# Kernel tuning notes

Measured on AMD Instinct MI355X. Metric: run time of the kernel, lower is better.

## Reference

```python
import jax, jax.numpy as jnp
import numpy as np

N = 8192
FEAT = 128
HID = 128
EMB = 128
NHEADS = 2
RO_HID = 256
G_EMB = 128
ALPHA = 0.2          # LeakyReLU negative slope
NEG_INF = -9e15      # matches -9000000000000000.0 in the torch source


def _xavier(k, shape, gain=1.0):
    fan_in, fan_out = shape[-2], shape[-1]
    s = gain * np.sqrt(2.0 / (fan_in + fan_out))
    return jax.random.normal(k, shape, jnp.float32) * jnp.float32(s)


def setup_inputs() -> dict:
    key = jax.random.key(0)
    ks = jax.random.split(key, 10)
    adj = jax.random.randint(ks[0], (N, N), 0, 2, jnp.int32)          # dense 0/1 adjacency
    x = jax.random.normal(ks[1], (N, FEAT), jnp.float32)
    W_heads = _xavier(ks[2], (NHEADS, FEAT, HID), gain=1.414)
    a_heads = _xavier(ks[3], (NHEADS, 2 * HID, 1), gain=1.414)
    W_out = _xavier(ks[4], (NHEADS * HID, EMB), gain=1.414)
    a_out = _xavier(ks[5], (2 * EMB, 1), gain=1.414)
    ge_w1 = _xavier(ks[6], (FEAT + EMB, RO_HID))
    ge_b1 = jnp.zeros((RO_HID,), jnp.float32)
    ge_w2 = _xavier(ks[7], (RO_HID, G_EMB))
    ge_b2 = jnp.zeros((G_EMB,), jnp.float32)
    return dict(adj=adj, feature_matrix=x, W_heads=W_heads, a_heads=a_heads,
                W_out=W_out, a_out=a_out, ge_w1=ge_w1, ge_b1=ge_b1,
                ge_w2=ge_w2, ge_b2=ge_b2, supply=0)


def _gat_layer(x, mask, W, a, concat):
    # Faithful to GraphAttentionLayer: e_ij = leakyrelu([Wh_i || Wh_j] @ a).
    # The concat-then-matmul decomposes exactly as Wh@a[:F] + (Wh@a[F:])^T,
    # avoiding the O(N^2 * 2F) a_input tensor while computing identical math.
    Wh = x @ W                                   # [N, F]
    F_out = W.shape[1]
    f1 = (Wh @ a[:F_out]).squeeze(-1)            # [N]
    f2 = (Wh @ a[F_out:]).squeeze(-1)            # [N]
    e = jax.nn.leaky_relu(f1[:, None] + f2[None, :], ALPHA)   # [N, N]
    e = jnp.where(mask, e, jnp.float32(NEG_INF))
    att = jax.nn.softmax(e, axis=1)              # dropout is identity in eval mode
    h = att @ Wh                                 # [N, F]
    return jax.nn.elu(h) if concat else h


def reference(adj, feature_matrix, W_heads, a_heads, W_out, a_out,
              ge_w1, ge_b1, ge_w2, ge_b2, supply):
    mask = adj > 0
    # GAT: multi-head layer 1 (concat), then out_att (no concat) + elu
    heads = [_gat_layer(feature_matrix, mask, W_heads[i], a_heads[i], True)
             for i in range(NHEADS)]
    h = jnp.concatenate(heads, axis=1)           # [N, NHEADS*HID]
    node_emb = jax.nn.elu(_gat_layer(h, mask, W_out, a_out, False))  # [N, EMB]
    # GraphEmb readout (mode='mean')
    combined = jnp.concatenate([feature_matrix, node_emb], axis=1)   # [N, FEAT+EMB]
    h1 = jax.nn.relu(combined @ ge_w1 + ge_b1)
    h2 = jax.nn.relu(h1 @ ge_w2 + ge_b2)
    graph_emb = jnp.mean(h2, axis=0)             # [G_EMB]
    return node_emb, graph_emb
```

## Files before the change

kernel.cpp:

```cpp
#include <hip/hip_runtime.h>

typedef unsigned short u16;
typedef __attribute__((ext_vector_type(4))) float f32x4;
typedef __attribute__((ext_vector_type(8))) short bf16x8;
typedef __attribute__((ext_vector_type(4))) unsigned short u16x4;
typedef __attribute__((ext_vector_type(4))) float float4v;

#define N 8192

__device__ __forceinline__ float bf2f(u16 u){
  union { float f; unsigned int i; } v; v.i = ((unsigned int)u) << 16; return v.f;
}
__device__ __forceinline__ u16 f2bf(float f){
  union { float f; unsigned int i; } v; v.f = f;
  unsigned int r = v.i + 0x7fffu + ((v.i >> 16) & 1u);
  return (u16)(r >> 16);
}
__device__ __forceinline__ f32x4 mfma16(bf16x8 a, bf16x8 b, f32x4 c){
  return __builtin_amdgcn_mfma_f32_16x16x32_bf16(a, b, c, 0, 0, 0);
}

__global__ __launch_bounds__(256) void k_pack(const int* __restrict__ adj,
                                              unsigned long long* __restrict__ packed){
  const int wid = blockIdx.x * 4 + (threadIdx.x >> 6);
  const int lane = threadIdx.x & 63;
  const size_t base = (size_t)wid * 128;
  for (int g = 0; g < 128; ++g){
    const size_t grp = base + g;
    const int v = adj[grp * 64 + lane];
    const unsigned long long mask = __ballot(v != 0);
    if (lane == 0) packed[grp] = mask;
  }
}

__global__ void k_split_x(const float* __restrict__ x, u16* __restrict__ hi, u16* __restrict__ lo){
  const int idx = blockIdx.x * 256 + threadIdx.x;
  float4v v = ((const float4v*)x)[idx];
  u16x4 h, l;
  #pragma unroll
  for (int e = 0; e < 4; ++e){ u16 hb = f2bf(v[e]); h[e] = hb; l[e] = f2bf(v[e] - bf2f(hb)); }
  ((u16x4*)hi)[idx] = h; ((u16x4*)lo)[idx] = l;
}

template<bool SPLIT>
__global__ void k_transpose(const float* __restrict__ src, u16* __restrict__ dhi,
                            u16* __restrict__ dlo, int K, int Ncols){
  const size_t boff = (size_t)blockIdx.y * K * Ncols;
  const int idx = blockIdx.x * 256 + threadIdx.x;
  if (idx >= K * Ncols) return;
  const int n = idx / K, k = idx % K;
  const float v = src[boff + (size_t)k * Ncols + n];
  const u16 h = f2bf(v);
  dhi[boff + idx] = h;
  if constexpr (SPLIT) dlo[boff + idx] = f2bf(v - bf2f(h));
}

__global__ __launch_bounds__(64) void k_gemm_at(
    const u16* __restrict__ Ahi, const u16* __restrict__ Alo,
    const u16* __restrict__ Bhi, const u16* __restrict__ Blo,
    u16* __restrict__ outT,
    const float* __restrict__ avec,
    float* __restrict__ f1, float* __restrict__ f2,
    int K)
{
  const int head = blockIdx.z;
  Ahi += (size_t)head * 128 * K; Alo += (size_t)head * 128 * K;
  outT += (size_t)head * 128 * N;
  avec += (size_t)head * 256;
  f1 += (size_t)head * N; f2 += (size_t)head * N;
  const int lane = threadIdx.x & 63;
  const int r16 = lane & 15, g4 = lane >> 4;
  const int cg = blockIdx.y;
  const size_t ib = (size_t)blockIdx.x * 128;
  f32x4 acc[8];
  #pragma unroll
  for (int it = 0; it < 8; ++it) acc[it] = (f32x4){0.f, 0.f, 0.f, 0.f};
  for (int kk = 0; kk < K; kk += 32){
    bf16x8 ah = *(const bf16x8*)(Ahi + (size_t)(cg * 16 + r16) * K + kk + g4 * 8);
    bf16x8 al = *(const bf16x8*)(Alo + (size_t)(cg * 16 + r16) * K + kk + g4 * 8);
    #pragma unroll
    for (int it = 0; it < 8; ++it){
      const size_t boff = (ib + it * 16 + r16) * (size_t)K + kk + g4 * 8;
      bf16x8 bh = *(const bf16x8*)(Bhi + boff);
      bf16x8 bl = *(const bf16x8*)(Blo + boff);
      acc[it] = mfma16(ah, bh, acc[it]);
      acc[it] = mfma16(ah, bl, acc[it]);
      acc[it] = mfma16(al, bh, acc[it]);
    }
  }
  float a1v[4], a2v[4];
  #pragma unroll
  for (int q = 0; q < 4; ++q){
    a1v[q] = avec[cg * 16 + g4 * 4 + q];
    a2v[q] = avec[128 + cg * 16 + g4 * 4 + q];
  }
  #pragma unroll
  for (int it = 0; it < 8; ++it){
    float p1 = 0.f, p2 = 0.f;
    #pragma unroll
    for (int q = 0; q < 4; ++q){
      float v = acc[it][q];
      outT[(size_t)(cg * 16 + g4 * 4 + q) * N + ib + it * 16 + r16] = f2bf(v);
      p1 += v * a1v[q]; p2 += v * a2v[q];
    }
    p1 += __shfl_xor(p1, 16); p1 += __shfl_xor(p1, 32);
    p2 += __shfl_xor(p2, 16); p2 += __shfl_xor(p2, 32);
    if (lane < 16){
      atomicAdd(&f1[ib + it * 16 + lane], p1);
      atomicAdd(&f2[ib + it * 16 + lane], p2);
    }
  }
}

template<int RG, bool L2OUT>
__global__ __launch_bounds__(256) void k_attn(
    const unsigned char* __restrict__ pk,
    const u16* __restrict__ whT_all,
    const float* __restrict__ f1_all, const float* __restrict__ f2_all,
    u16* __restrict__ out_hi, u16* __restrict__ out_lo,
    float* __restrict__ out_f32, u16* __restrict__ comb)
{
  constexpr int ROWS = RG * 16;
  __shared__ float smO[3][ROWS][132];
  __shared__ float smM[3][ROWS];
  __shared__ float smL[3][ROWS];

  const int h = blockIdx.y;
  const u16* whT = whT_all + (size_t)h * 128 * N;
  const float* f1 = f1_all + (size_t)h * N;
  const float* f2 = f2_all + (size_t)h * N;
  const int seg = threadIdx.x >> 6;
  const int lane = threadIdx.x & 63;
  const int r16 = lane & 15, g4 = lane >> 4;
  const size_t ibase = (size_t)blockIdx.x * ROWS;

  float m[RG], l[RG], f1v[RG];
  f32x4 acc[RG][8];
  #pragma unroll
  for (int rg = 0; rg < RG; ++rg){
    m[rg] = -3e38f; l[rg] = 0.f;
    f1v[rg] = f1[ibase + rg * 16 + r16];
    #pragma unroll
    for (int ct = 0; ct < 8; ++ct) acc[rg][ct] = (f32x4){0.f, 0.f, 0.f, 0.f};
  }

  for (int t = seg; t < 128; t += 4){
    const int j0 = t * 64;
    bf16x8 bfr[2][8];
    #pragma unroll
    for (int kk = 0; kk < 2; ++kk)
      #pragma unroll
      for (int ct = 0; ct < 8; ++ct)
        bfr[kk][ct] = *(const bf16x8*)(whT + (size_t)(ct * 16 + r16) * N + j0 + kk * 32 + g4 * 8);
    float4v f2a = *(const float4v*)(f2 + j0 + g4 * 8);
    float4v f2b = *(const float4v*)(f2 + j0 + g4 * 8 + 4);
    float4v f2c = *(const float4v*)(f2 + j0 + 32 + g4 * 8);
    float4v f2d = *(const float4v*)(f2 + j0 + 32 + g4 * 8 + 4);
    float f2v[16] = {f2a[0],f2a[1],f2a[2],f2a[3], f2b[0],f2b[1],f2b[2],f2b[3],
                     f2c[0],f2c[1],f2c[2],f2c[3], f2d[0],f2d[1],f2d[2],f2d[3]};
    unsigned int bits[RG][2];
    #pragma unroll
    for (int rg = 0; rg < RG; ++rg){
      const size_t rb = (ibase + rg * 16 + r16) * 1024 + (j0 >> 3);
      bits[rg][0] = pk[rb + g4];
      bits[rg][1] = pk[rb + 4 + g4];
    }
    #pragma unroll
    for (int rg = 0; rg < RG; ++rg){
      float e[16]; float tmax = -3e38f;
      #pragma unroll
      for (int kk = 0; kk < 2; ++kk)
        #pragma unroll
        for (int x = 0; x < 8; ++x){
          float s = f1v[rg] + f2v[kk * 8 + x];
          s = (s > 0.f) ? s : 0.2f * s;
          s = ((bits[rg][kk] >> x) & 1u) ? s : -3e38f;
          e[kk * 8 + x] = s; tmax = fmaxf(tmax, s);
        }
      tmax = fmaxf(tmax, __shfl_xor(tmax, 16));
      tmax = fmaxf(tmax, __shfl_xor(tmax, 32));
      const float mold = m[rg];
      const float mnew = fmaxf(mold, tmax);
      m[rg] = mnew;
      float psum = 0.f;
      u16 pb[16];
      #pragma unroll
      for (int kk = 0; kk < 2; ++kk)
        #pragma unroll
        for (int x = 0; x < 8; ++x){
          float p = ((bits[rg][kk] >> x) & 1u) ? __expf(e[kk * 8 + x] - mnew) : 0.f;
          psum += p;
          pb[kk * 8 + x] = f2bf(p);
        }
      psum += __shfl_xor(psum, 16);
      psum += __shfl_xor(psum, 32);
      const float sc = __expf(mold - mnew);
      l[rg] = l[rg] * sc + psum;
      if (__any(mnew != mold)){
        float s0 = __shfl(sc, g4 * 4 + 0), s1 = __shfl(sc, g4 * 4 + 1);
        float s2 = __shfl(sc, g4 * 4 + 2), s3 = __shfl(sc, g4 * 4 + 3);
        f32x4 sv = {s0, s1, s2, s3};
        #pragma unroll
        for (int ct = 0; ct < 8; ++ct) acc[rg][ct] *= sv;
      }
      bf16x8 a0, a1;
      #pragma unroll
      for (int x = 0; x < 8; ++x){ a0[x] = (short)pb[x]; a1[x] = (short)pb[8 + x]; }
      #pragma unroll
      for (int ct = 0; ct < 8; ++ct){
        acc[rg][ct] = mfma16(a0, bfr[0][ct], acc[rg][ct]);
        acc[rg][ct] = mfma16(a1, bfr[1][ct], acc[rg][ct]);
      }
    }
  }
  if (seg > 0){
    #pragma unroll
    for (int rg = 0; rg < RG; ++rg){
      #pragma unroll
      for (int ct = 0; ct < 8; ++ct)
        #pragma unroll
        for (int q = 0; q < 4; ++q)
          smO[seg - 1][rg * 16 + g4 * 4 + q][ct * 16 + r16] = acc[rg][ct][q];
      if (lane < 16){ smM[seg - 1][rg * 16 + lane] = m[rg]; smL[seg - 1][rg * 16 + lane] = l[rg]; }
    }
  }
  __syncthreads();
  if (seg == 0){
    #pragma unroll
    for (int rg = 0; rg < RG; ++rg){
      #pragma unroll
      for (int q = 0; q < 4; ++q){
        const int r = rg * 16 + g4 * 4 + q;
        const float m0 = __shfl(m[rg], g4 * 4 + q);
        const float l0 = __shfl(l[rg], g4 * 4 + q);
        const float mm = fmaxf(fmaxf(m0, smM[0][r]), fmaxf(smM[1][r], smM[2][r]));
        const float w0 = __expf(m0 - mm);
        const float w1 = __expf(smM[0][r] - mm);
        const float w2 = __expf(smM[1][r] - mm);
        const float w3 = __expf(smM[2][r] - mm);
        const float L = w0 * l0 + w1 * smL[0][r] + w2 * smL[1][r] + w3 * smL[2][r];
        const float rinv = 1.f / L;
        #pragma unroll
        for (int ct = 0; ct < 8; ++ct){
          const int c = ct * 16 + r16;
          float val = w0 * acc[rg][ct][q] + w1 * smO[0][r][c] + w2 * smO[1][r][c] + w3 * smO[2][r][c];
          float o = val * rinv;
          o = (o > 0.f) ? o : (__expf(o) - 1.f);
          const size_t i = ibase + r;
          if constexpr (!L2OUT){
            const u16 hb = f2bf(o);
            out_hi[i * 256 + (size_t)h * 128 + c] = hb;
            out_lo[i * 256 + (size_t)h * 128 + c] = f2bf(o - bf2f(hb));
          } else {
            out_f32[i * 128 + c] = o;
            comb[i * 256 + 128 + c] = f2bf(o);
          }
        }
      }
    }
  }
}

__global__ void k_copyx(const float* __restrict__ x, u16* __restrict__ comb){
  const int idx = blockIdx.x * 256 + threadIdx.x;
  const int i = idx >> 5;
  const int c4 = (idx & 31) * 4;
  float4v v = *(const float4v*)(x + (size_t)i * 128 + c4);
  u16x4 hv;
  #pragma unroll
  for (int e = 0; e < 4; ++e) hv[e] = f2bf(v[e]);
  *(u16x4*)(comb + (size_t)i * 256 + c4) = hv;
}

template<bool STORE, bool COLSUM>
__global__ __launch_bounds__(256) void k_gemm_row(
    const u16* __restrict__ A,
    const u16* __restrict__ BT,
    const float* __restrict__ bias,
    u16* __restrict__ out, float* __restrict__ csum,
    int K, int Ntot)
{
  const int lane = threadIdx.x & 63, w = threadIdx.x >> 6;
  const int r16 = lane & 15, g4 = lane >> 4;
  const size_t rbase = (size_t)blockIdx.x * 64 + w * 16;
  const int cbase = blockIdx.y * 128;
  f32x4 acc[8];
  #pragma unroll
  for (int ct = 0; ct < 8; ++ct) acc[ct] = (f32x4){0.f, 0.f, 0.f, 0.f};
  for (int kk = 0; kk < K; kk += 32){
    bf16x8 af = *(const bf16x8*)(A + (rbase + r16) * (size_t)K + kk + g4 * 8);
    #pragma unroll
    for (int ct = 0; ct < 8; ++ct){
      bf16x8 bfr = *(const bf16x8*)(BT + (size_t)(cbase + ct * 16 + r16) * K + kk + g4 * 8);
      acc[ct] = mfma16(af, bfr, acc[ct]);
    }
  }
  #pragma unroll
  for (int ct = 0; ct < 8; ++ct){
    const float bv = bias[cbase + ct * 16 + r16];
    float s = 0.f;
    #pragma unroll
    for (int q = 0; q < 4; ++q){
      float v = acc[ct][q] + bv;
      v = fmaxf(v, 0.f);
      if constexpr (STORE)
        out[(rbase + g4 * 4 + q) * (size_t)Ntot + cbase + ct * 16 + r16] = f2bf(v);
      s += v;
    }
    if constexpr (COLSUM){
      s += __shfl_xor(s, 16); s += __shfl_xor(s, 32);
      if (lane < 16) atomicAdd(&csum[cbase + ct * 16 + lane], s);
    }
  }
}

__global__ void k_final(const float* __restrict__ csum, float* __restrict__ out){
  out[threadIdx.x] = csum[threadIdx.x] * (1.f / 8192.f);
}

extern "C" void kernel_launch(void* const* d_in, const int* in_sizes, int n_in,
                              void* d_out, int out_size, void* d_ws, size_t ws_size,
                              hipStream_t stream) {
  const int*   adj = (const int*)d_in[0];
  const float* x   = (const float*)d_in[1];
  const float* Wh  = (const float*)d_in[2];
  const float* ah  = (const float*)d_in[3];
  const float* Wo  = (const float*)d_in[4];
  const float* ao  = (const float*)d_in[5];
  const float* g1  = (const float*)d_in[6];
  const float* b1  = (const float*)d_in[7];
  const float* g2  = (const float*)d_in[8];
  const float* b2  = (const float*)d_in[9];
  float* outp = (float*)d_out;
  char* ws = (char*)d_ws;

  const size_t PK   = 0;
  const size_t WHT1 = 8388608;
  const size_t FV   = 12582912;
  const size_t F1A  = FV;
  const size_t F2A  = FV + 65536;
  const size_t F1B  = FV + 131072;
  const size_t F2B  = FV + 163840;
  const size_t HHI  = 12779520;
  const size_t HLO  = 16973824;
  const size_t WHT2 = 21168128;
  const size_t XHI  = 23265280;
  const size_t XLO  = 25362432;
  const size_t CSUM = 27459584;
  const size_t WTHH = 27460096;
  const size_t WTHL = 27525632;
  const size_t WOTH = 27591168;
  const size_t WOTL = 27656704;
  const size_t G1T  = 27722240;
  const size_t G2T  = 27853312;
  const size_t H1   = PK;
  const size_t COMB = WHT1;

  hipMemsetAsync(ws + FV, 0, 196608, stream);
  hipMemsetAsync(ws + CSUM, 0, 512, stream);

  k_pack<<<2048, 256, 0, stream>>>(adj, (unsigned long long*)(ws + PK));
  k_split_x<<<1024, 256, 0, stream>>>(x, (u16*)(ws + XHI), (u16*)(ws + XLO));
  k_transpose<true ><<<dim3(64, 2), 256, 0, stream>>>(Wh, (u16*)(ws + WTHH), (u16*)(ws + WTHL), 128, 128);
  k_transpose<true ><<<dim3(128, 1), 256, 0, stream>>>(Wo, (u16*)(ws + WOTH), (u16*)(ws + WOTL), 256, 128);
  k_transpose<false><<<dim3(256, 1), 256, 0, stream>>>(g1, (u16*)(ws + G1T), nullptr, 256, 256);
  k_transpose<false><<<dim3(128, 1), 256, 0, stream>>>(g2, (u16*)(ws + G2T), nullptr, 256, 128);

  k_gemm_at<<<dim3(64, 8, 2), 64, 0, stream>>>(
      (const u16*)(ws + WTHH), (const u16*)(ws + WTHL),
      (const u16*)(ws + XHI),  (const u16*)(ws + XLO),
      (u16*)(ws + WHT1), ah, (float*)(ws + F1A), (float*)(ws + F2A), 128);

  k_attn<2, false><<<dim3(256, 2), 256, 0, stream>>>(
      (const unsigned char*)(ws + PK), (const u16*)(ws + WHT1),
      (const float*)(ws + F1A), (const float*)(ws + F2A),
      (u16*)(ws + HHI), (u16*)(ws + HLO), nullptr, nullptr);

  k_gemm_at<<<dim3(64, 8, 1), 64, 0, stream>>>(
      (const u16*)(ws + WOTH), (const u16*)(ws + WOTL),
      (const u16*)(ws + HHI),  (const u16*)(ws + HLO),
      (u16*)(ws + WHT2), ao, (float*)(ws + F1B), (float*)(ws + F2B), 256);

  k_copyx<<<1024, 256, 0, stream>>>(x, (u16*)(ws + COMB));

  k_attn<1, true><<<dim3(512, 1), 256, 0, stream>>>(
      (const unsigned char*)(ws + PK), (const u16*)(ws + WHT2),
      (const float*)(ws + F1B), (const float*)(ws + F2B),
      nullptr, nullptr, outp, (u16*)(ws + COMB));

  k_gemm_row<true, false><<<dim3(128, 2), 256, 0, stream>>>(
      (const u16*)(ws + COMB), (const u16*)(ws + G1T), b1,
      (u16*)(ws + H1), nullptr, 256, 256);
  k_gemm_row<false, true><<<dim3(128, 1), 256, 0, stream>>>(
      (const u16*)(ws + H1), (const u16*)(ws + G2T), b2,
      nullptr, (float*)(ws + CSUM), 256, 128);
  k_final<<<1, 128, 0, stream>>>((const float*)(ws + CSUM), outp + (size_t)N * 128);
}
```

Before: 811.0 us.

## Use static softmax max bound, split-K attention with merge, drop hi/lo bf16 split

Attention logits are now computed as x·(W a) through small GEMV kernels in a log2 scale. The per-row softmax maximum is taken as an upper bound from leakyrelu(f1 + max f2), which removes online max tracking and accumulator rescaling. Attention is split over key segments across many small 64-thread blocks, and each segment writes bf16 partial outputs and row sums that a separate merge kernel combines, applying normalization and ELU. The hi/lo split bf16 GEMMs are replaced by plain bf16. This raises parallelism and removes the rescale work, but adds partial-buffer memory traffic, extra launches, and some loss of precision.

```diff
diff --git a/kernel.cpp b/kernel.cpp
--- a/kernel.cpp
+++ b/kernel.cpp
@@ -1,12 +1,13 @@
 #include <hip/hip_runtime.h>
+#include <hip/hip_bf16.h>
 
 typedef unsigned short u16;
 typedef __attribute__((ext_vector_type(4))) float f32x4;
 typedef __attribute__((ext_vector_type(8))) short bf16x8;
 typedef __attribute__((ext_vector_type(4))) unsigned short u16x4;
-typedef __attribute__((ext_vector_type(4))) float float4v;
 
 #define N 8192
+#define LOG2E 1.4426950408889634f
 
 __device__ __forceinline__ float bf2f(u16 u){
   union { float f; unsigned int i; } v; v.i = ((unsigned int)u) << 16; return v.f;
@@ -25,6 +26,7 @@
   const int wid = blockIdx.x * 4 + (threadIdx.x >> 6);
   const int lane = threadIdx.x & 63;
   const size_t base = (size_t)wid * 128;
+  #pragma unroll 4
   for (int g = 0; g < 128; ++g){
     const size_t grp = base + g;
     const int v = adj[grp * 64 + lane];
@@ -33,249 +35,280 @@
   }
 }
 
-__global__ void k_split_x(const float* __restrict__ x, u16* __restrict__ hi, u16* __restrict__ lo){
+__global__ __launch_bounds__(256) void k_x2bf(const float* __restrict__ x,
+                                              u16* __restrict__ xbf, u16* __restrict__ comb){
   const int idx = blockIdx.x * 256 + threadIdx.x;
-  float4v v = ((const float4v*)x)[idx];
-  u16x4 h, l;
-  #pragma unroll
-  for (int e = 0; e < 4; ++e){ u16 hb = f2bf(v[e]); h[e] = hb; l[e] = f2bf(v[e] - bf2f(hb)); }
-  ((u16x4*)hi)[idx] = h; ((u16x4*)lo)[idx] = l;
-}
-
-template<bool SPLIT>
-__global__ void k_transpose(const float* __restrict__ src, u16* __restrict__ dhi,
-                            u16* __restrict__ dlo, int K, int Ncols){
+  f32x4 v = ((const f32x4*)x)[idx];
+  u16x4 h;
+  #pragma unroll
+  for (int e = 0; e < 4; ++e) h[e] = f2bf(v[e]);
+  ((u16x4*)xbf)[idx] = h;
+  const int i = idx >> 5, c4 = (idx & 31) * 4;
+  *(u16x4*)(comb + (size_t)i * 256 + c4) = h;
+}
+
+__global__ void k_transpose(const float* __restrict__ src, u16* __restrict__ dst,
+                            int K, int Ncols){
   const size_t boff = (size_t)blockIdx.y * K * Ncols;
   const int idx = blockIdx.x * 256 + threadIdx.x;
   if (idx >= K * Ncols) return;
   const int n = idx / K, k = idx % K;
-  const float v = src[boff + (size_t)k * Ncols + n];
-  const u16 h = f2bf(v);
-  dhi[boff + idx] = h;
-  if constexpr (SPLIT) dlo[boff + idx] = f2bf(v - bf2f(h));
-}
-
-__global__ __launch_bounds__(64) void k_gemm_at(
-    const u16* __restrict__ Ahi, const u16* __restrict__ Alo,
-    const u16* __restrict__ Bhi, const u16* __restrict__ Blo,
-    u16* __restrict__ outT,
-    const float* __restrict__ avec,
-    float* __restrict__ f1, float* __restrict__ f2,
-    int K)
-{
-  const int head = blockIdx.z;
-  Ahi += (size_t)head * 128 * K; Alo += (size_t)head * 128 * K;
-  outT += (size_t)head * 128 * N;
-  avec += (size_t)head * 256;
-  f1 += (size_t)head * N; f2 += (size_t)head * N;
-  const int lane = threadIdx.x & 63;
+  dst[boff + idx] = f2bf(src[boff + (size_t)k * Ncols + n]);
+}
+
+__global__ __launch_bounds__(256) void k_wa(const float* __restrict__ Wh, const float* __restrict__ ah,
+                                            const float* __restrict__ Wo, const float* __restrict__ ao,
+                                            float* __restrict__ wa){
+  const int z = blockIdx.x, t = threadIdx.x;
+  if (z < 2){
+    if (t < 128){
+      float a1 = 0.f, a2 = 0.f;
+      for (int c = 0; c < 128; ++c){
+        const float w = Wh[(size_t)z * 16384 + t * 128 + c];
+        a1 += w * ah[z * 256 + c];
+        a2 += w * ah[z * 256 + 128 + c];
+      }
+      wa[z * 128 + t] = a1; wa[256 + z * 128 + t] = a2;
+    }
+  } else {
+    if (t < 256){
+      float a1 = 0.f, a2 = 0.f;
+      for (int c = 0; c < 128; ++c){
+        const float w = Wo[(size_t)t * 128 + c];
+        a1 += w * ao[c];
+        a2 += w * ao[128 + c];
+      }
+      wa[512 + t] = a1; wa[768 + t] = a2;
+    }
+  }
+}
+
+__global__ __launch_bounds__(256) void k_gemv1(const float* __restrict__ x, const float* __restrict__ wa,
+                                               float* __restrict__ f1s, float* __restrict__ f2s){
+  const int h = blockIdx.y;
+  const float* wa1 = wa + h * 128;
+  const float* wa2 = wa + 256 + h * 128;
+  const int lane = threadIdx.x & 63, w = threadIdx.x >> 6;
   const int r16 = lane & 15, g4 = lane >> 4;
-  const int cg = blockIdx.y;
-  const size_t ib = (size_t)blockIdx.x * 128;
-  f32x4 acc[8];
-  #pragma unroll
-  for (int it = 0; it < 8; ++it) acc[it] = (f32x4){0.f, 0.f, 0.f, 0.f};
+  const int row = blockIdx.x * 16 + w * 4 + g4;
+  const float* xr = x + (size_t)row * 128 + r16 * 8;
+  f32x4 x0 = *(const f32x4*)(xr);
+  f32x4 x1 = *(const f32x4*)(xr + 4);
+  f32x4 wA0 = *(const f32x4*)(wa1 + r16 * 8);
+  f32x4 wA1 = *(const f32x4*)(wa1 + r16 * 8 + 4);
+  f32x4 wB0 = *(const f32x4*)(wa2 + r16 * 8);
+  f32x4 wB1 = *(const f32x4*)(wa2 + r16 * 8 + 4);
+  float d1 = 0.f, d2 = 0.f;
+  #pragma unroll
+  for (int e = 0; e < 4; ++e){
+    d1 += x0[e] * wA0[e] + x1[e] * wA1[e];
+    d2 += x0[e] * wB0[e] + x1[e] * wB1[e];
+  }
+  d1 += __shfl_xor(d1, 1); d1 += __shfl_xor(d1, 2); d1 += __shfl_xor(d1, 4); d1 += __shfl_xor(d1, 8);
+  d2 += __shfl_xor(d2, 1); d2 += __shfl_xor(d2, 2); d2 += __shfl_xor(d2, 4); d2 += __shfl_xor(d2, 8);
+  if (r16 == 0){
+    f1s[(size_t)h * N + row] = d1 * LOG2E;
+    f2s[(size_t)h * N + row] = d2 * LOG2E;
+  }
+}
+
+__global__ __launch_bounds__(256) void k_gemv2(const u16* __restrict__ hbf,
+                                               const float* __restrict__ wao1, const float* __restrict__ wao2,
+                                               float* __restrict__ f1s, float* __restrict__ f2s){
+  const int lane = threadIdx.x & 63, w = threadIdx.x >> 6;
+  const int r16 = lane & 15, g4 = lane >> 4;
+  const int row = blockIdx.x * 16 + w * 4 + g4;
+  bf16x8 h0 = *(const bf16x8*)(hbf + (size_t)row * 256 + r16 * 16);
+  bf16x8 h1 = *(const bf16x8*)(hbf + (size_t)row * 256 + r16 * 16 + 8);
+  float d1 = 0.f, d2 = 0.f;
+  #pragma unroll
+  for (int e = 0; e < 8; ++e){
+    const float v0 = bf2f((u16)h0[e]), v1 = bf2f((u16)h1[e]);
+    d1 += v0 * wao1[r16 * 16 + e] + v1 * wao1[r16 * 16 + 8 + e];
+    d2 += v0 * wao2[r16 * 16 + e] + v1 * wao2[r16 * 16 + 8 + e];
+  }
+  d1 += __shfl_xor(d1, 1); d1 += __shfl_xor(d1, 2); d1 += __shfl_xor(d1, 4); d1 += __shfl_xor(d1, 8);
+  d2 += __shfl_xor(d2, 1); d2 += __shfl_xor(d2, 2); d2 += __shfl_xor(d2, 4); d2 += __shfl_xor(d2, 8);
+  if (r16 == 0){
+    f1s[row] = d1 * LOG2E;
+    f2s[row] = d2 * LOG2E;
+  }
+}
+
+__global__ __launch_bounds__(256) void k_fmax(const float* __restrict__ f2s, float* __restrict__ fmax){
+  const int h = blockIdx.x;
+  const float* f = f2s + (size_t)h * N;
+  float m = -3e38f;
+  for (int i = threadIdx.x; i < N; i += 256) m = fmaxf(m, f[i]);
+  m = fmaxf(m, __shfl_xor(m, 1));  m = fmaxf(m, __shfl_xor(m, 2));
+  m = fmaxf(m, __shfl_xor(m, 4));  m = fmaxf(m, __shfl_xor(m, 8));
+  m = fmaxf(m, __shfl_xor(m, 16)); m = fmaxf(m, __shfl_xor(m, 32));
+  __shared__ float sm[4];
+  if ((threadIdx.x & 63) == 0) sm[threadIdx.x >> 6] = m;
+  __syncthreads();
+  if (threadIdx.x == 0) fmax[h] = fmaxf(fmaxf(sm[0], sm[1]), fmaxf(sm[2], sm[3]));
+}
+
+__global__ __launch_bounds__(256) void k_gemm_at(const u16* __restrict__ A_all, const u16* __restrict__ B,
+                                                 u16* __restrict__ outT_all, int K){
+  const int head = blockIdx.y;
+  const u16* A = A_all + (size_t)head * 128 * K;
+  u16* outT = outT_all + (size_t)head * 128 * N;
+  const int lane = threadIdx.x & 63, w = threadIdx.x >> 6;
+  const int r16 = lane & 15, g4 = lane >> 4;
+  const size_t ib = (size_t)blockIdx.x * 128 + w * 32;
+  f32x4 acc[8][2];
+  #pragma unroll
+  for (int cg = 0; cg < 8; ++cg){ acc[cg][0] = (f32x4){0,0,0,0}; acc[cg][1] = (f32x4){0,0,0,0}; }
   for (int kk = 0; kk < K; kk += 32){
-    bf16x8 ah = *(const bf16x8*)(Ahi + (size_t)(cg * 16 + r16) * K + kk + g4 * 8);
-    bf16x8 al = *(const bf16x8*)(Alo + (size_t)(cg * 16 + r16) * K + kk + g4 * 8);
-    #pragma unroll
-    for (int it = 0; it < 8; ++it){
-      const size_t boff = (ib + it * 16 + r16) * (size_t)K + kk + g4 * 8;
-      bf16x8 bh = *(const bf16x8*)(Bhi + boff);
-      bf16x8 bl = *(const bf16x8*)(Blo + boff);
-      acc[it] = mfma16(ah, bh, acc[it]);
-      acc[it] = mfma16(ah, bl, acc[it]);
-      acc[it] = mfma16(al, bh, acc[it]);
-    }
-  }
-  float a1v[4], a2v[4];
-  #pragma unroll
-  for (int q = 0; q < 4; ++q){
-    a1v[q] = avec[cg * 16 + g4 * 4 + q];
-    a2v[q] = avec[128 + cg * 16 + g4 * 4 + q];
-  }
-  #pragma unroll
-  for (int it = 0; it < 8; ++it){
-    float p1 = 0.f, p2 = 0.f;
-    #pragma unroll
-    for (int q = 0; q < 4; ++q){
-      float v = acc[it][q];
-      outT[(size_t)(cg * 16 + g4 * 4 + q) * N + ib + it * 16 + r16] = f2bf(v);
-      p1 += v * a1v[q]; p2 += v * a2v[q];
-    }
-    p1 += __shfl_xor(p1, 16); p1 += __shfl_xor(p1, 32);
-    p2 += __shfl_xor(p2, 16); p2 += __shfl_xor(p2, 32);
-    if (lane < 16){
-      atomicAdd(&f1[ib + it * 16 + lane], p1);
-      atomicAdd(&f2[ib + it * 16 + lane], p2);
-    }
-  }
-}
-
-template<int RG, bool L2OUT>
-__global__ __launch_bounds__(256) void k_attn(
+    bf16x8 b0 = *(const bf16x8*)(B + (ib + r16) * (size_t)K + kk + g4 * 8);
+    bf16x8 b1 = *(const bf16x8*)(B + (ib + 16 + r16) * (size_t)K + kk + g4 * 8);
+    #pragma unroll
+    for (int cg = 0; cg < 8; ++cg){
+      bf16x8 a = *(const bf16x8*)(A + (size_t)(cg * 16 + r16) * K + kk + g4 * 8);
+      acc[cg][0] = mfma16(a, b0, acc[cg][0]);
+      acc[cg][1] = mfma16(a, b1, acc[cg][1]);
+    }
+  }
+  #pragma unroll
+  for (int cg = 0; cg < 8; ++cg)
+    #pragma unroll
+    for (int it = 0; it < 2; ++it)
+      #pragma unroll
+      for (int q = 0; q < 4; ++q)
+        outT[(size_t)(cg * 16 + g4 * 4 + q) * N + ib + it * 16 + r16] = f2bf(acc[cg][it][q]);
+}
+
+template<int S>
+__global__ __launch_bounds__(64, 3) void k_attn(
     const unsigned char* __restrict__ pk,
     const u16* __restrict__ whT_all,
     const float* __restrict__ f1_all, const float* __restrict__ f2_all,
-    u16* __restrict__ out_hi, u16* __restrict__ out_lo,
-    float* __restrict__ out_f32, u16* __restrict__ comb)
+    const float* __restrict__ fmax_all,
+    u16* __restrict__ part, float* __restrict__ pl)
 {
-  constexpr int ROWS = RG * 16;
-  __shared__ float smO[3][ROWS][132];
-  __shared__ float smM[3][ROWS];
-  __shared__ float smL[3][ROWS];
-
-  const int h = blockIdx.y;
+  const int h = blockIdx.z;
+  const int s = blockIdx.y;
   const u16* whT = whT_all + (size_t)h * 128 * N;
   const float* f1 = f1_all + (size_t)h * N;
   const float* f2 = f2_all + (size_t)h * N;
-  const int seg = threadIdx.x >> 6;
-  const int lane = threadIdx.x & 63;
+  const float fmax = fmax_all[h];
+  const int lane = threadIdx.x;
   const int r16 = lane & 15, g4 = lane >> 4;
-  const size_t ibase = (size_t)blockIdx.x * ROWS;
-
-  float m[RG], l[RG], f1v[RG];
-  f32x4 acc[RG][8];
-  #pragma unroll
-  for (int rg = 0; rg < RG; ++rg){
-    m[rg] = -3e38f; l[rg] = 0.f;
+  const size_t ibase = (size_t)blockIdx.x * 32;
+  const int t0 = (s * 128) / S, t1 = ((s + 1) * 128) / S;
+
+  float f1v[2], mrow[2], lsum[2];
+  f32x4 acc[2][8];
+  #pragma unroll
+  for (int rg = 0; rg < 2; ++rg){
     f1v[rg] = f1[ibase + rg * 16 + r16];
-    #pragma unroll
-    for (int ct = 0; ct < 8; ++ct) acc[rg][ct] = (f32x4){0.f, 0.f, 0.f, 0.f};
-  }
-
-  for (int t = seg; t < 128; t += 4){
+    const float v = f1v[rg] + fmax;
+    mrow[rg] = fmaxf(v, 0.2f * v);
+    lsum[rg] = 0.f;
+    #pragma unroll
+    for (int ct = 0; ct < 8; ++ct) acc[rg][ct] = (f32x4){0,0,0,0};
+  }
+
+  for (int t = t0; t < t1; ++t){
     const int j0 = t * 64;
-    bf16x8 bfr[2][8];
-    #pragma unroll
-    for (int kk = 0; kk < 2; ++kk)
-      #pragma unroll
-      for (int ct = 0; ct < 8; ++ct)
-        bfr[kk][ct] = *(const bf16x8*)(whT + (size_t)(ct * 16 + r16) * N + j0 + kk * 32 + g4 * 8);
-    float4v f2a = *(const float4v*)(f2 + j0 + g4 * 8);
-    float4v f2b = *(const float4v*)(f2 + j0 + g4 * 8 + 4);
-    float4v f2c = *(const float4v*)(f2 + j0 + 32 + g4 * 8);
-    float4v f2d = *(const float4v*)(f2 + j0 + 32 + g4 * 8 + 4);
-    float f2v[16] = {f2a[0],f2a[1],f2a[2],f2a[3], f2b[0],f2b[1],f2b[2],f2b[3],
-                     f2c[0],f2c[1],f2c[2],f2c[3], f2d[0],f2d[1],f2d[2],f2d[3]};
-    unsigned int bits[RG][2];
-    #pragma unroll
-    for (int rg = 0; rg < RG; ++rg){
-      const size_t rb = (ibase + rg * 16 + r16) * 1024 + (j0 >> 3);
+    float fs[16];
+    *(f32x4*)&fs[0]  = *(const f32x4*)(f2 + j0 + g4 * 8);
+    *(f32x4*)&fs[4]  = *(const f32x4*)(f2 + j0 + g4 * 8 + 4);
+    *(f32x4*)&fs[8]  = *(const f32x4*)(f2 + j0 + 32 + g4 * 8);
+    *(f32x4*)&fs[12] = *(const f32x4*)(f2 + j0 + 32 + g4 * 8 + 4);
+    unsigned int bits[2][2];
+    #pragma unroll
+    for (int rg = 0; rg < 2; ++rg){
+      const size_t rb = (ibase + rg * 16 + r16) * 1024 + t * 8;
       bits[rg][0] = pk[rb + g4];
       bits[rg][1] = pk[rb + 4 + g4];
     }
-    #pragma unroll
-    for (int rg = 0; rg < RG; ++rg){
-      float e[16]; float tmax = -3e38f;
+    bf16x8 pa[2][2];
+    #pragma unroll
+    for (int rg = 0; rg < 2; ++rg){
       #pragma unroll
-      for (int kk = 0; kk < 2; ++kk)
+      for (int k2 = 0; k2 < 2; ++k2){
+        float pv[8];
         #pragma unroll
         for (int x = 0; x < 8; ++x){
-          float s = f1v[rg] + f2v[kk * 8 + x];
-          s = (s > 0.f) ? s : 0.2f * s;
-          s = ((bits[rg][kk] >> x) & 1u) ? s : -3e38f;
-          e[kk * 8 + x] = s; tmax = fmaxf(tmax, s);
+          const float y = f1v[rg] + fs[k2 * 8 + x];
+          const float lr = fmaxf(y, 0.2f * y);
+          const float p = exp2f(lr - mrow[rg]);
+          pv[x] = ((bits[rg][k2] >> x) & 1u) ? p : 0.f;
+          lsum[rg] += pv[x];
         }
-      tmax = fmaxf(tmax, __shfl_xor(tmax, 16));
-      tmax = fmaxf(tmax, __shfl_xor(tmax, 32));
-      const float mold = m[rg];
-      const float mnew = fmaxf(mold, tmax);
-      m[rg] = mnew;
-      float psum = 0.f;
-      u16 pb[16];
-      #pragma unroll
-      for (int kk = 0; kk < 2; ++kk)
-        #pragma unroll
-        for (int x = 0; x < 8; ++x){
-          float p = ((bits[rg][kk] >> x) & 1u) ? __expf(e[kk * 8 + x] - mnew) : 0.f;
-          psum += p;
-          pb[kk * 8 + x] = f2bf(p);
-        }
-      psum += __shfl_xor(psum, 16);
-      psum += __shfl_xor(psum, 32);
-      const float sc = __expf(mold - mnew);
-      l[rg] = l[rg] * sc + psum;
-      if (__any(mnew != mold)){
-        float s0 = __shfl(sc, g4 * 4 + 0), s1 = __shfl(sc, g4 * 4 + 1);
-        float s2 = __shfl(sc, g4 * 4 + 2), s3 = __shfl(sc, g4 * 4 + 3);
-        f32x4 sv = {s0, s1, s2, s3};
-        #pragma unroll
-        for (int ct = 0; ct < 8; ++ct) acc[rg][ct] *= sv;
+        union { __hip_bfloat162 h2[4]; bf16x8 v8; } u;
+        u.h2[0] = __float22bfloat162_rn(make_float2(pv[0], pv[1]));
+        u.h2[1] = __float22bfloat162_rn(make_float2(pv[2], pv[3]));
+        u.h2[2] = __float22bfloat162_rn(make_float2(pv[4], pv[5]));
+        u.h2[3] = __float22bfloat162_rn(make_float2(pv[6], pv[7]));
+        pa[rg][k2] = u.v8;
       }
-      bf16x8 a0, a1;
-      #pragma unroll
-      for (int x = 0; x < 8; ++x){ a0[x] = (short)pb[x]; a1[x] = (short)pb[8 + x]; }
+    }
+    #pragma unroll
+    for (int k2 = 0; k2 < 2; ++k2){
       #pragma unroll
       for (int ct = 0; ct < 8; ++ct){
-        acc[rg][ct] = mfma16(a0, bfr[0][ct], acc[rg][ct]);
-        acc[rg][ct] = mfma16(a1, bfr[1][ct], acc[rg][ct]);
+        bf16x8 b = *(const bf16x8*)(whT + (size_t)(ct * 16 + r16) * N + j0 + k2 * 32 + g4 * 8);
+        acc[0][ct] = mfma16(pa[0][k2], b, acc[0][ct]);
+        acc[1][ct] = mfma16(pa[1][k2], b, acc[1][ct]);
       }
     }
   }
-  if (seg > 0){
-    #pragma unroll
-    for (int rg = 0; rg < RG; ++rg){
+
+  const int plane = h * S + s;
+  u16* pp = part + (size_t)plane * (size_t)N * 128;
+  #pragma unroll
+  for (int rg = 0; rg < 2; ++rg){
+    float lv = lsum[rg];
+    lv += __shfl_xor(lv, 16); lv += __shfl_xor(lv, 32);
+    if (lane < 16) pl[(size_t)plane * N + ibase + rg * 16 + lane] = lv;
+    #pragma unroll
+    for (int ct = 0; ct < 8; ++ct)
       #pragma unroll
-      for (int ct = 0; ct < 8; ++ct)
-        #pragma unroll
-        for (int q = 0; q < 4; ++q)
-          smO[seg - 1][rg * 16 + g4 * 4 + q][ct * 16 + r16] = acc[rg][ct][q];
-      if (lane < 16){ smM[seg - 1][rg * 16 + lane] = m[rg]; smL[seg - 1][rg * 16 + lane] = l[rg]; }
-    }
-  }
-  __syncthreads();
-  if (seg == 0){
-    #pragma unroll
-    for (int rg = 0; rg < RG; ++rg){
-      #pragma unroll
-      for (int q = 0; q < 4; ++q){
-        const int r = rg * 16 + g4 * 4 + q;
-        const float m0 = __shfl(m[rg], g4 * 4 + q);
-        const float l0 = __shfl(l[rg], g4 * 4 + q);
-        const float mm = fmaxf(fmaxf(m0, smM[0][r]), fmaxf(smM[1][r], smM[2][r]));
-        const float w0 = __expf(m0 - mm);
-        const float w1 = __expf(smM[0][r] - mm);
-        const float w2 = __expf(smM[1][r] - mm);
-        const float w3 = __expf(smM[2][r] - mm);
-        const float L = w0 * l0 + w1 * smL[0][r] + w2 * smL[1][r] + w3 * smL[2][r];
-        const float rinv = 1.f / L;
-        #pragma unroll
-        for (int ct = 0; ct < 8; ++ct){
-          const int c = ct * 16 + r16;
-          float val = w0 * acc[rg][ct][q] + w1 * smO[0][r][c] + w2 * smO[1][r][c] + w3 * smO[2][r][c];
-          float o = val * rinv;
-          o = (o > 0.f) ? o : (__expf(o) - 1.f);
-          const size_t i = ibase + r;
-          if constexpr (!L2OUT){
-            const u16 hb = f2bf(o);
-            out_hi[i * 256 + (size_t)h * 128 + c] = hb;
-            out_lo[i * 256 + (size_t)h * 128 + c] = f2bf(o - bf2f(hb));
-          } else {
-            out_f32[i * 128 + c] = o;
-            comb[i * 256 + 128 + c] = f2bf(o);
-          }
-        }
-      }
-    }
-  }
-}
-
-__global__ void k_copyx(const float* __restrict__ x, u16* __restrict__ comb){
+      for (int q = 0; q < 4; ++q)
+        pp[(ibase + rg * 16 + g4 * 4 + q) * 128 + ct * 16 + r16] = f2bf(acc[rg][ct][q]);
+  }
+}
+
+template<int S, bool L2>
+__global__ __launch_bounds__(256) void k_attn_merge(
+    const u16* __restrict__ part, const float* __restrict__ pl,
+    u16* __restrict__ hbf, float* __restrict__ nodeout, u16* __restrict__ comb)
+{
+  const int h = blockIdx.y;
   const int idx = blockIdx.x * 256 + threadIdx.x;
-  const int i = idx >> 5;
-  const int c4 = (idx & 31) * 4;
-  float4v v = *(const float4v*)(x + (size_t)i * 128 + c4);
+  const int i = idx >> 5, c4 = (idx & 31) * 4;
+  f32x4 a = (f32x4){0,0,0,0};
+  float L = 0.f;
+  #pragma unroll
+  for (int s = 0; s < S; ++s){
+    const size_t plane = h * S + s;
+    u16x4 v = *(const u16x4*)(part + plane * (size_t)N * 128 + (size_t)i * 128 + c4);
+    a[0] += bf2f(v[0]); a[1] += bf2f(v[1]); a[2] += bf2f(v[2]); a[3] += bf2f(v[3]);
+    L += pl[plane * (size_t)N + i];
+  }
+  const float linv = 1.f / L;
   u16x4 hv;
   #pragma unroll
-  for (int e = 0; e < 4; ++e) hv[e] = f2bf(v[e]);
-  *(u16x4*)(comb + (size_t)i * 256 + c4) = hv;
+  for (int e = 0; e < 4; ++e){
+    float o = a[e] * linv;
+    o = (o > 0.f) ? o : (__expf(o) - 1.f);
+    a[e] = o;
+    hv[e] = f2bf(o);
+  }
+  if constexpr (!L2){
+    *(u16x4*)(hbf + (size_t)i * 256 + h * 128 + c4) = hv;
+  } else {
+    *(f32x4*)(nodeout + (size_t)i * 128 + c4) = a;
+    *(u16x4*)(comb + (size_t)i * 256 + 128 + c4) = hv;
+  }
 }
 
 template<bool STORE, bool COLSUM>
 __global__ __launch_bounds__(256) void k_gemm_row(
-    const u16* __restrict__ A,
-    const u16* __restrict__ BT,
+    const u16* __restrict__ A, const u16* __restrict__ BT,
     const float* __restrict__ bias,
     u16* __restrict__ out, float* __restrict__ csum,
     int K, int Ntot)
@@ -286,7 +319,7 @@
   const int cbase = blockIdx.y * 128;
   f32x4 acc[8];
   #pragma unroll
-  for (int ct = 0; ct < 8; ++ct) acc[ct] = (f32x4){0.f, 0.f, 0.f, 0.f};
+  for (int ct = 0; ct < 8; ++ct) acc[ct] = (f32x4){0,0,0,0};
   for (int kk = 0; kk < K; kk += 32){
     bf16x8 af = *(const bf16x8*)(A + (rbase + r16) * (size_t)K + kk + g4 * 8);
     #pragma unroll
@@ -298,18 +331,18 @@
   #pragma unroll
   for (int ct = 0; ct < 8; ++ct){
     const float bv = bias[cbase + ct * 16 + r16];
-    float s = 0.f;
+    float sacc = 0.f;
     #pragma unroll
     for (int q = 0; q < 4; ++q){
       float v = acc[ct][q] + bv;
       v = fmaxf(v, 0.f);
       if constexpr (STORE)
         out[(rbase + g4 * 4 + q) * (size_t)Ntot + cbase + ct * 16 + r16] = f2bf(v);
-      s += v;
+      sacc += v;
     }
     if constexpr (COLSUM){
-      s += __shfl_xor(s, 16); s += __shfl_xor(s, 32);
-      if (lane < 16) atomicAdd(&csum[cbase + ct * 16 + lane], s);
+      sacc += __shfl_xor(sacc, 16); sacc += __shfl_xor(sacc, 32);
+      if (lane < 16) atomicAdd(&csum[cbase + ct * 16 + lane], sacc);
     }
   }
 }
@@ -334,65 +367,67 @@
   float* outp = (float*)d_out;
   char* ws = (char*)d_ws;
 
-  const size_t PK   = 0;
-  const size_t WHT1 = 8388608;
-  const size_t FV   = 12582912;
-  const size_t F1A  = FV;
-  const size_t F2A  = FV + 65536;
-  const size_t F1B  = FV + 131072;
-  const size_t F2B  = FV + 163840;
-  const size_t HHI  = 12779520;
-  const size_t HLO  = 16973824;
-  const size_t WHT2 = 21168128;
-  const size_t XHI  = 23265280;
-  const size_t XLO  = 25362432;
-  const size_t CSUM = 27459584;
-  const size_t WTHH = 27460096;
-  const size_t WTHL = 27525632;
-  const size_t WOTH = 27591168;
-  const size_t WOTL = 27656704;
-  const size_t G1T  = 27722240;
-  const size_t G2T  = 27853312;
-  const size_t H1   = PK;
-  const size_t COMB = WHT1;
-
-  hipMemsetAsync(ws + FV, 0, 196608, stream);
+  constexpr size_t PK   = 0;
+  constexpr size_t PART = 8388608;
+  constexpr size_t PL   = 33554432;
+  constexpr size_t XBF  = 33947648;
+  constexpr size_t WHT1 = 36044800;
+  constexpr size_t WHT2 = 40239104;
+  constexpr size_t HBF  = 42336256;
+  constexpr size_t COMB = 46530560;
+  constexpr size_t H1RO = 50724864;
+  constexpr size_t F1S  = 54919168;
+  constexpr size_t F2S  = 54984704;
+  constexpr size_t FMAX = 55050240;
+  constexpr size_t CSUM = 55050496;
+  constexpr size_t WTH  = 55051008;
+  constexpr size_t WOT  = 55116544;
+  constexpr size_t G1T  = 55182080;
+  constexpr size_t G2T  = 55313152;
+  constexpr size_t WA   = 55378688;
+
   hipMemsetAsync(ws + CSUM, 0, 512, stream);
 
   k_pack<<<2048, 256, 0, stream>>>(adj, (unsigned long long*)(ws + PK));
-  k_split_x<<<1024, 256, 0, stream>>>(x, (u16*)(ws + XHI), (u16*)(ws + XLO));
-  k_transpose<true ><<<dim3(64, 2), 256, 0, stream>>>(Wh, (u16*)(ws + WTHH), (u16*)(ws + WTHL), 128, 128);
-  k_transpose<true ><<<dim3(128, 1), 256, 0, stream>>>(Wo, (u16*)(ws + WOTH), (u16*)(ws + WOTL), 256, 128);
-  k_transpose<false><<<dim3(256, 1), 256, 0, stream>>>(g1, (u16*)(ws + G1T), nullptr, 256, 256);
-  k_transpose<false><<<dim3(128, 1), 256, 0, stream>>>(g2, (u16*)(ws + G2T), nullptr, 256, 128);
-
-  k_gemm_at<<<dim3(64, 8, 2), 64, 0, stream>>>(
-      (const u16*)(ws + WTHH), (const u16*)(ws + WTHL),
-      (const u16*)(ws + XHI),  (const u16*)(ws + XLO),
-      (u16*)(ws + WHT1), ah, (float*)(ws + F1A), (float*)(ws + F2A), 128);
-
-  k_attn<2, false><<<dim3(256, 2), 256, 0, stream>>>(
+  k_x2bf<<<1024, 256, 0, stream>>>(x, (u16*)(ws + XBF), (u16*)(ws + COMB));
+  k_transpose<<<dim3(64, 2), 256, 0, stream>>>(Wh, (u16*)(ws + WTH), 128, 128);
+  k_transpose<<<dim3(128, 1), 256, 0, stream>>>(Wo, (u16*)(ws + WOT), 256, 128);
+  k_transpose<<<dim3(256, 1), 256, 0, stream>>>(g1, (u16*)(ws + G1T), 256, 256);
+  k_transpose<<<dim3(128, 1), 256, 0, stream>>>(g2, (u16*)(ws + G2T), 256, 128);
+  k_wa<<<3, 256, 0, stream>>>(Wh, ah, Wo, ao, (float*)(ws + WA));
+
+  k_gemv1<<<dim3(512, 2), 256, 0, stream>>>(x, (const float*)(ws + WA),
+                                            (float*)(ws + F1S), (float*)(ws + F2S));
+  k_fmax<<<2, 256, 0, stream>>>((const float*)(ws + F2S), (float*)(ws + FMAX));
+  k_gemm_at<<<dim3(64, 2), 256, 0, stream>>>((const u16*)(ws + WTH), (const u16*)(ws + XBF),
+                                             (u16*)(ws + WHT1), 128);
+  k_attn<6><<<dim3(256, 6, 2), 64, 0, stream>>>(
       (const unsigned char*)(ws + PK), (const u16*)(ws + WHT1),
-      (const float*)(ws + F1A), (const float*)(ws + F2A),
-      (u16*)(ws + HHI), (u16*)(ws + HLO), nullptr, nullptr);
-
-  k_gemm_at<<<dim3(64, 8, 1), 64, 0, stream>>>(
-      (const u16*)(ws + WOTH), (const u16*)(ws + WOTL),
-      (const u16*)(ws + HHI),  (const u16*)(ws + HLO),
-      (u16*)(ws + WHT2), ao, (float*)(ws + F1B), (float*)(ws + F2B), 256);
-
-  k_copyx<<<1024, 256, 0, stream>>>(x, (u16*)(ws + COMB));
-
-  k_attn<1, true><<<dim3(512, 1), 256, 0, stream>>>(
+      (const float*)(ws + F1S), (const float*)(ws + F2S), (const float*)(ws + FMAX),
+      (u16*)(ws + PART), (float*)(ws + PL));
+  k_attn_merge<6, false><<<dim3(1024, 2), 256, 0, stream>>>(
+      (const u16*)(ws + PART), (const float*)(ws + PL),
+      (u16*)(ws + HBF), nullptr, nullptr);
+
+  k_gemv2<<<dim3(512, 1), 256, 0, stream>>>((const u16*)(ws + HBF),
+      (const float*)(ws + WA) + 512, (const float*)(ws + WA) + 768,
+      (float*)(ws + F1S), (float*)(ws + F2S));
+  k_fmax<<<1, 256, 0, stream>>>((const float*)(ws + F2S), (float*)(ws + FMAX));
+  k_gemm_at<<<dim3(64, 1), 256, 0, stream>>>((const u16*)(ws + WOT), (const u16*)(ws + HBF),
+                                             (u16*)(ws + WHT2), 256);
+  k_attn<12><<<dim3(256, 12, 1), 64, 0, stream>>>(
       (const unsigned char*)(ws + PK), (const u16*)(ws + WHT2),
-      (const float*)(ws + F1B), (const float*)(ws + F2B),
-      nullptr, nullptr, outp, (u16*)(ws + COMB));
+      (const float*)(ws + F1S), (const float*)(ws + F2S), (const float*)(ws + FMAX),
+      (u16*)(ws + PART), (float*)(ws + PL));
+  k_attn_merge<12, true><<<dim3(1024, 1), 256, 0, stream>>>(
+      (const u16*)(ws + PART), (const float*)(ws + PL),
+      nullptr, outp, (u16*)(ws + COMB));
 
   k_gemm_row<true, false><<<dim3(128, 2), 256, 0, stream>>>(
       (const u16*)(ws + COMB), (const u16*)(ws + G1T), b1,
-      (u16*)(ws + H1), nullptr, 256, 256);
+      (u16*)(ws + H1RO), nullptr, 256, 256);
   k_gemm_row<false, true><<<dim3(128, 1), 256, 0, stream>>>(
-      (const u16*)(ws + H1), (const u16*)(ws + G2T), b2,
+      (const u16*)(ws + H1RO), (const u16*)(ws + G2T), b2,
       nullptr, (float*)(ws + CSUM), 256, 128);
   k_final<<<1, 128, 0, stream>>>((const float*)(ws + CSUM), outp + (size_t)N * 128);
 }
```

After: 768.3 us. 5.3% less time.
